# Kernel optimization log

Measured on AMD Instinct MI355X. Metric: run time of the kernel, lower is better.

The kernel has to match this reference:

```python
import jax, jax.numpy as jnp
import numpy as np

B, S, IN_DIM, OUT_DIM = 4, 2048, 1024, 1024
NEG = -9e15

def _xavier(key, shape, gain=1.414):
    fan_in, fan_out = shape[0], shape[1]
    a = gain * np.sqrt(6.0 / (fan_in + fan_out))
    return jax.random.uniform(key, shape, jnp.float32, -a, a)

def setup_inputs() -> dict:
    key = jax.random.key(0)
    ks = jax.random.split(key, 8)
    x = jax.random.normal(ks[0], (B, S, IN_DIM), jnp.float32)
    W_query = _xavier(ks[1], (IN_DIM, OUT_DIM))
    W_key = _xavier(ks[2], (IN_DIM, OUT_DIM))
    W_value = _xavier(ks[3], (IN_DIM, OUT_DIM))
    # torch Linear default init (kaiming-uniform-ish); values don't matter for correctness baseline
    W1 = _xavier(ks[4], (OUT_DIM + IN_DIM, OUT_DIM), gain=1.0)
    b1 = jnp.zeros((OUT_DIM,), jnp.float32)
    W2 = _xavier(ks[5], (OUT_DIM, OUT_DIM), gain=1.0)
    b2 = jnp.zeros((OUT_DIM,), jnp.float32)
    return {"x": x, "W_query": W_query, "W_key": W_key, "W_value": W_value,
            "W1": W1, "b1": b1, "W2": W2, "b2": b2}

def reference(x, W_query, W_key, W_value, W1, b1, W2, b2):
    # QKV projections: [B,S,in] @ [in,out] -> [B,S,out]
    q = jnp.einsum('bsi,io->bso', x, W_query)
    k = jnp.einsum('bsi,io->bso', x, W_key)
    v = jnp.einsum('bsi,io->bso', x, W_value)
    scale = 1.0 / jnp.sqrt(jnp.float32(OUT_DIM))
    e = jnp.einsum('bqd,bkd->bqk', q, k) * scale  # [B,S,S]
    causal = jnp.tril(jnp.ones((S, S), jnp.float32))  # mask > 0 keeps lower triangle
    attn = jnp.where(causal > 0, e, jnp.float32(NEG))
    attn = jax.nn.softmax(attn, axis=2)
    # dropout: eval mode (train=False) -> identity
    out = jnp.einsum('bqk,bkd->bqd', attn, v)  # [B,S,out]
    h = jnp.concatenate([out, x], axis=-1)  # [B,S,out+in]
    h = jax.nn.relu(jnp.einsum('bsf,fo->bso', h, W1) + b1)
    return jnp.einsum('bsf,fo->bso', h, W2) + b2
```

## Files before the change

kernel.cpp:

```cpp
#include <hip/hip_runtime.h>
#include <stdint.h>

typedef __attribute__((ext_vector_type(8))) short short8;
typedef __attribute__((ext_vector_type(4))) float f32x4;

__device__ __forceinline__ unsigned short f32_to_bf16(float f) {
    unsigned int u = __float_as_uint(f);
    u += 0x7FFFu + ((u >> 16) & 1u);
    return (unsigned short)(u >> 16);
}

__device__ __forceinline__ short8 load8_f32_as_bf16(const float* __restrict__ ap) {
    f32x4 f0 = *(const f32x4*)ap;
    f32x4 f1 = *(const f32x4*)(ap + 4);
    union { short8 s; unsigned short u[8]; } cv;
#pragma unroll
    for (int t = 0; t < 4; ++t) {
        cv.u[t]     = f32_to_bf16(f0[t]);
        cv.u[t + 4] = f32_to_bf16(f1[t]);
    }
    return cv.s;
}

__device__ __forceinline__ void gld_lds16(const void* g, void* l) {
    __builtin_amdgcn_global_load_lds(
        (const __attribute__((address_space(1))) unsigned int*)(unsigned long long)(uintptr_t)g,
        (__attribute__((address_space(3))) unsigned int*)(unsigned int)(uintptr_t)l,
        16, 0, 0);
}

__device__ __forceinline__ int triC(int y) {
    int t = y >> 1;
    return y + t * (t - 1) + ((y & 1) ? t : 0);
}

template<int AMODE, int EPI, int SWIZ, bool KLIMIT, int MT>
__global__ __launch_bounds__(256, 4)
void gemm128(const unsigned short* __restrict__ A, const unsigned short* __restrict__ A2,
             int lda, int lda2, int ksplit,
             const unsigned short* __restrict__ B, int ldb,
             void* __restrict__ C, int ldc, int K,
             long aStride, long bStride, long cStride,
             const float* __restrict__ bias, long biasStride, float scale,
             void* __restrict__ C2, int ldc2)
{
    int z = blockIdx.z;
    int mblk, nblk;
    if (SWIZ == 1) {
        int lin = blockIdx.y * gridDim.x + blockIdx.x;
        int mchunk = gridDim.y >> 3;
        int xcd = lin & 7, idx = lin >> 3;
        mblk = xcd * mchunk + idx % mchunk;
        nblk = idx / mchunk;
    } else if (SWIZ == 4) {
        mblk = (z & 2) ? ((int)gridDim.y - 1 - (int)blockIdx.y) : blockIdx.y;
        nblk = blockIdx.x;
    } else if (SWIZ == 5) {
        int x = blockIdx.x;
        int a = (int)(2.f * sqrtf((float)x));
        if (a > 31) a = 31;
        while (a < 31 && triC(a + 1) <= x) ++a;
        while (a > 0 && triC(a) > x) --a;
        mblk = a;
        nblk = x - triC(a);
    } else if (SWIZ == 6) {
        int x = blockIdx.x, yy = blockIdx.y;
        if (z < 2) { mblk = x * 8 + (yy & 7); nblk = yy >> 3; }
        else       { nblk = x * 8 + (yy & 7); mblk = yy >> 3; }
    } else {
        mblk = blockIdx.y;
        nblk = blockIdx.x;
    }
    int m0 = mblk * MT;
    int n0 = nblk * 128;

    const unsigned short* Ab;
    const unsigned short* Bb;
    if (SWIZ == 6) {
        if (z < 2) { Ab = A; Bb = B + (size_t)z * bStride; }
        else       { Ab = B + (size_t)2 * bStride; Bb = A; }
    } else {
        Ab = A + (size_t)z * aStride;
        Bb = B + (size_t)z * bStride;
    }

    __shared__ __align__(16) short As[MT * 64];
    __shared__ __align__(16) short Bs[128 * 64];

    int tid  = threadIdx.x;
    int lane = tid & 63, wid = tid >> 6;
    constexpr int MI = MT / 32;
    int wm = (wid & 1) * (MT / 2), wn = (wid >> 1) * 64;
    int fr = lane & 15, fq = lane >> 4;
    int sw0 = ((fq    ) ^ (fr & 7)) * 16;
    int sw1 = ((fq ^ 4) ^ (fr & 7)) * 16;

    int rS = tid >> 3;
    int cS = ((tid & 7) ^ (rS & 7)) * 8;
    char* AsB = (char*)As; char* BsB = (char*)Bs;

    int kend = KLIMIT ? min(K, m0 + MT) : K;

    f32x4 acc[MI][4];
#pragma unroll
    for (int i = 0; i < MI; ++i)
#pragma unroll
    for (int j = 0; j < 4; ++j) acc[i][j] = f32x4{0.f, 0.f, 0.f, 0.f};

    for (int k0 = 0; k0 < kend; k0 += 64) {
        const unsigned short* Asrc = Ab;
        int koff = k0, ldax = lda;
        if (AMODE == 2 && k0 >= ksplit) { Asrc = A2; koff = k0 - ksplit; ldax = lda2; }
        const unsigned short* pa = Asrc + (size_t)(m0 + rS) * ldax + koff + cS;
        const unsigned short* pb = Bb   + (size_t)(n0 + rS) * ldb  + k0   + cS;
#pragma unroll
        for (int t = 0; t < MT / 32; ++t)
            gld_lds16(pa + (size_t)(32 * t) * ldax, AsB + t * 4096 + tid * 16);
#pragma unroll
        for (int t = 0; t < 4; ++t)
            gld_lds16(pb + (size_t)(32 * t) * ldb,  BsB + t * 4096 + tid * 16);
        __syncthreads();

#pragma unroll
        for (int kh = 0; kh < 2; ++kh) {
            int sw = kh ? sw1 : sw0;
            short8 a[MI], b[4];
#pragma unroll
            for (int i = 0; i < MI; ++i)
                a[i] = *(const short8*)(AsB + (wm + i * 16 + fr) * 128 + sw);
#pragma unroll
            for (int j = 0; j < 4; ++j)
                b[j] = *(const short8*)(BsB + (wn + j * 16 + fr) * 128 + sw);
#pragma unroll
            for (int i = 0; i < MI; ++i)
#pragma unroll
            for (int j = 0; j < 4; ++j)
                acc[i][j] = __builtin_amdgcn_mfma_f32_16x16x32_bf16(a[i], b[j], acc[i][j], 0, 0, 0);
        }
        __syncthreads();
    }

    if (EPI == 0) {
        unsigned short* Cz; int ldcz;
        if (SWIZ == 6 && z >= 2) { Cz = (unsigned short*)C2; ldcz = ldc2; }
        else { Cz = (unsigned short*)C + (size_t)z * cStride; ldcz = ldc; }
#pragma unroll
        for (int i = 0; i < MI; ++i)
#pragma unroll
        for (int j = 0; j < 4; ++j)
#pragma unroll
        for (int r = 0; r < 4; ++r) {
            int row = m0 + wm + i * 16 + fq * 4 + r;
            int col = n0 + wn + j * 16 + fr;
            Cz[(size_t)row * ldcz + col] = f32_to_bf16(acc[i][j][r]);
        }
    } else if (EPI == 6) {
        unsigned short* Cz = (unsigned short*)C + (size_t)z * cStride;
        float* rs = const_cast<float*>(bias) + z * biasStride;
#pragma unroll
        for (int i = 0; i < MI; ++i)
#pragma unroll
        for (int r = 0; r < 4; ++r) {
            int row = m0 + wm + i * 16 + fq * 4 + r;
            float s = 0.f;
#pragma unroll
            for (int j = 0; j < 4; ++j) {
                int col = n0 + wn + j * 16 + fr;
                float e = (col <= row) ? __expf(acc[i][j][r] * scale - 16.f) : 0.f;
                s += e;
                Cz[(size_t)row * ldc + col] = f32_to_bf16(e);
            }
            s += __shfl_xor(s, 1);
            s += __shfl_xor(s, 2);
            s += __shfl_xor(s, 4);
            s += __shfl_xor(s, 8);
            if (fr == 0) atomicAdd(&rs[row], s);
        }
    } else if (EPI == 4) {
        unsigned short* Cz = (unsigned short*)C + (size_t)z * cStride;
#pragma unroll
        for (int i = 0; i < MI; ++i)
#pragma unroll
        for (int r = 0; r < 4; ++r) {
            int row = m0 + wm + i * 16 + fq * 4 + r;
            float inv = 1.f / bias[z * biasStride + row];
#pragma unroll
            for (int j = 0; j < 4; ++j) {
                int col = n0 + wn + j * 16 + fr;
                Cz[(size_t)row * ldc + col] = f32_to_bf16(acc[i][j][r] * inv);
            }
        }
    } else {
#pragma unroll
        for (int i = 0; i < MI; ++i)
#pragma unroll
        for (int j = 0; j < 4; ++j)
#pragma unroll
        for (int r = 0; r < 4; ++r) {
            int row = m0 + wm + i * 16 + fq * 4 + r;
            int col = n0 + wn + j * 16 + fr;
            float v = acc[i][j][r];
            if (EPI == 2) {
                v += bias[col];
                v = v > 0.f ? v : 0.f;
                ((unsigned short*)C + (size_t)z * cStride)[(size_t)row * ldc + col] = f32_to_bf16(v);
            } else {
                ((float*)C + (size_t)z * cStride)[(size_t)row * ldc + col] = v + bias[col];
            }
        }
    }
}

__device__ __forceinline__ void transpose_tile32(const float* __restrict__ in,
                                                 unsigned short* __restrict__ out,
                                                 int rows, int cols, int bx, int by, int tid)
{
    __shared__ float t[32][33];
    int tx = tid & 31, ty = tid >> 5;
    int r0 = by * 32, c0 = bx * 32;
#pragma unroll
    for (int i = 0; i < 4; ++i)
        t[ty + i * 8][tx] = in[(size_t)(r0 + ty + i * 8) * cols + c0 + tx];
    __syncthreads();
#pragma unroll
    for (int i = 0; i < 4; ++i)
        out[(size_t)(c0 + ty + i * 8) * rows + r0 + tx] = f32_to_bf16(t[tx][ty + i * 8]);
}

__global__ __launch_bounds__(256)
void prep_kernel(const float* __restrict__ x,
                 const float* __restrict__ Wq, const float* __restrict__ Wk,
                 const float* __restrict__ Wv, const float* __restrict__ W1,
                 const float* __restrict__ W2,
                 unsigned short* __restrict__ xb, unsigned short* __restrict__ WT,
                 unsigned short* __restrict__ W1T, unsigned short* __restrict__ W2T,
                 float* __restrict__ rsum)
{
    int idx = blockIdx.x;
    int tid = threadIdx.x;
    if (idx < 4096) {
        size_t i = ((size_t)idx * 256 + tid) * 8;
        *(short8*)(xb + i) = load8_f32_as_bf16(x + i);
    } else if (idx < 7168) {
        int t = idx - 4096;
        int w = t >> 10; t &= 1023;
        const float* in = w == 0 ? Wq : (w == 1 ? Wk : Wv);
        transpose_tile32(in, WT + (size_t)w * 1024 * 1024, 1024, 1024,
                         t & 31, t >> 5, tid);
    } else if (idx < 9216) {
        int t = idx - 7168;
        transpose_tile32(W1, W1T, 2048, 1024, t & 31, t >> 5, tid);
    } else if (idx < 10240) {
        int t = idx - 9216;
        transpose_tile32(W2, W2T, 1024, 1024, t & 31, t >> 5, tid);
    } else {
        int t = idx - 10240;
        f32x4 zero = {0.f, 0.f, 0.f, 0.f};
        float* p = rsum + ((size_t)t * 256 + tid) * 8;
        *(f32x4*)p = zero;
        *(f32x4*)(p + 4) = zero;
    }
}

extern "C" void kernel_launch(void* const* d_in, const int* in_sizes, int n_in,
                              void* d_out, int out_size, void* d_ws, size_t ws_size,
                              hipStream_t stream)
{
    const float* x  = (const float*)d_in[0];
    const float* Wq = (const float*)d_in[1];
    const float* Wk = (const float*)d_in[2];
    const float* Wv = (const float*)d_in[3];
    const float* W1 = (const float*)d_in[4];
    const float* b1 = (const float*)d_in[5];
    const float* W2 = (const float*)d_in[6];
    const float* b2 = (const float*)d_in[7];
    float* out = (float*)d_out;

    size_t off = 0;
    auto alloc = [&](size_t bytes) {
        char* r = (char*)d_ws + off;
        off += (bytes + 255) & ~(size_t)255;
        return r;
    };
    const size_t TOK = (size_t)8192 * 1024;
    unsigned short* WT   = (unsigned short*)alloc((size_t)3072 * 1024 * 2);
    unsigned short* W1T  = (unsigned short*)alloc((size_t)1024 * 2048 * 2);
    unsigned short* W2T  = (unsigned short*)alloc((size_t)1024 * 1024 * 2);
    unsigned short* xb   = (unsigned short*)alloc(TOK * 2);
    unsigned short* vT   = (unsigned short*)alloc((size_t)1024 * 8192 * 2);
    unsigned short* attn = (unsigned short*)alloc(TOK * 2);
    float*          rsum = (float*)         alloc((size_t)4 * 2048 * 4);
    unsigned short* q    = (unsigned short*)alloc(TOK * 2);
    unsigned short* k    = (unsigned short*)alloc(TOK * 2);
    unsigned short* S    = (unsigned short*)alloc((size_t)4 * 2048 * 2048 * 2);
    unsigned short* h1   = S;

    prep_kernel<<<10244, 256, 0, stream>>>(x, Wq, Wk, Wv, W1, W2, xb, WT, W1T, W2T, rsum);

    gemm128<0, 0, 6, false, 128><<<dim3(8, 64, 3), 256, 0, stream>>>(
        xb, nullptr, 1024, 0, 0, WT, 1024, q, 1024, 1024,
        0, (long)1024 * 1024, (long)TOK, nullptr, 0, 0.f, vT, 8192);

    gemm128<0, 6, 5, false, 64><<<dim3(272, 1, 4), 256, 0, stream>>>(
        q, nullptr, 1024, 0, 0, k, 1024, S, 2048, 1024,
        (long)2048 * 1024, (long)2048 * 1024, (long)2048 * 2048, rsum, 2048, 0.03125f,
        nullptr, 0);
    gemm128<0, 4, 4, true, 64><<<dim3(8, 32, 4), 256, 0, stream>>>(
        S, nullptr, 2048, 0, 0, vT, 8192, attn, 1024, 2048,
        (long)2048 * 2048, (long)2048, (long)2048 * 1024, rsum, 2048, 0.f, nullptr, 0);

    gemm128<2, 2, 1, false, 64><<<dim3(8, 128, 1), 256, 0, stream>>>(
        attn, xb, 1024, 1024, 1024, W1T, 2048, h1, 1024, 2048, 0, 0, 0, b1, 0, 0.f,
        nullptr, 0);
    gemm128<0, 3, 1, false, 64><<<dim3(8, 128, 1), 256, 0, stream>>>(
        h1, nullptr, 1024, 0, 0, W2T, 1024, out, 1024, 1024, 0, 0, 0, b2, 0, 0.f,
        nullptr, 0);
}
```

Before: 291.8 us.

## Add 256x128 eight-wave triple-buffered GEMM for QKV and MLP projections

Adds a new GEMM kernel with 512 threads, a 256x128 output tile and a three-slot LDS ring. Prefetch runs two K-steps ahead with one barrier per step, and setprio is raised around the MFMA block. The QKV projection and both MLP GEMMs now use it in place of the 128-tile kernel. The larger tile cuts global reloads and barrier overhead per FLOP, but it uses much more LDS, which may lower occupancy, and it leaves fewer blocks per grid.

```diff
diff --git a/kernel.cpp b/kernel.cpp
--- a/kernel.cpp
+++ b/kernel.cpp
@@ -211,6 +211,159 @@
     }
 }
 
+template<int AMODE, int EPI, int SWIZ>
+__global__ __launch_bounds__(512, 2)
+void gemm8p(const unsigned short* __restrict__ A, const unsigned short* __restrict__ A2,
+            int lda, int lda2, int ksplit,
+            const unsigned short* __restrict__ B, int ldb,
+            void* __restrict__ C, int ldc, int K,
+            long bStride, long cStride,
+            const float* __restrict__ bias,
+            void* __restrict__ C2, int ldc2)
+{
+    constexpr int BM = 256, BN = 128;
+    int z = blockIdx.z;
+    int lin = blockIdx.y * gridDim.x + blockIdx.x;
+    int xcd = lin & 7, idx = lin >> 3;
+    int mblk, nblk;
+    if (SWIZ == 6) {
+        if (z < 2) { mblk = xcd * 4 + (idx & 3); nblk = idx >> 2; }
+        else       { nblk = xcd * 8 + (idx & 7); mblk = idx >> 3; }
+    } else {
+        int mch = (int)gridDim.y >> 3;
+        mblk = xcd * mch + idx % mch;
+        nblk = idx / mch;
+    }
+    int m0 = mblk * BM, n0 = nblk * BN;
+
+    const unsigned short *Ab, *Bb;
+    if (SWIZ == 6) {
+        if (z < 2) { Ab = A; Bb = B + (size_t)z * bStride; }
+        else       { Ab = B + (size_t)2 * bStride; Bb = A; }
+    } else { Ab = A; Bb = B; }
+
+    constexpr int ATILE = BM * 64;
+    constexpr int BTILE = BN * 64;
+    constexpr int TILE  = ATILE + BTILE;
+    __shared__ __align__(16) short lds[3 * TILE];
+
+    int tid  = threadIdx.x;
+    int lane = tid & 63, wid = tid >> 6;
+    int wm = (wid & 3) * 64, wn = (wid >> 2) * 64;
+    int fr = lane & 15, fq = lane >> 4;
+    int sw0 = ((fq    ) ^ (fr & 7)) * 16;
+    int sw1 = ((fq ^ 4) ^ (fr & 7)) * 16;
+
+    int rS = tid >> 3;
+    int cS = ((tid & 7) ^ (rS & 7)) * 8;
+
+    int NT = K >> 6;
+
+    f32x4 acc[4][4];
+#pragma unroll
+    for (int i = 0; i < 4; ++i)
+#pragma unroll
+    for (int j = 0; j < 4; ++j) acc[i][j] = f32x4{0.f, 0.f, 0.f, 0.f};
+
+    auto STAGE = [&](int t, int slot) {
+        int k0 = t << 6;
+        char* dst = (char*)(lds + slot * TILE);
+        const unsigned short* Asrc = Ab; int koff = k0, ldax = lda;
+        if (AMODE == 2 && k0 >= ksplit) { Asrc = A2; koff = k0 - ksplit; ldax = lda2; }
+        const unsigned short* pa = Asrc + (size_t)(m0 + rS) * ldax + koff + cS;
+        const unsigned short* pb = Bb   + (size_t)(n0 + rS) * ldb  + k0   + cS;
+#pragma unroll
+        for (int u = 0; u < 4; ++u)
+            gld_lds16(pa + (size_t)(64 * u) * ldax, dst + u * 8192 + tid * 16);
+#pragma unroll
+        for (int u = 0; u < 2; ++u)
+            gld_lds16(pb + (size_t)(64 * u) * ldb, dst + 32768 + u * 8192 + tid * 16);
+    };
+
+    STAGE(0, 0);
+    STAGE(1, 1);
+    asm volatile("s_waitcnt vmcnt(6)" ::: "memory");
+    __builtin_amdgcn_s_barrier();
+    __builtin_amdgcn_sched_barrier(0);
+    asm volatile("" ::: "memory");
+
+    int sc = 0, ss = 2;
+    for (int t = 0; t < NT; ++t) {
+        if (t + 2 < NT) STAGE(t + 2, ss);
+        const char* AsB = (const char*)(lds + sc * TILE);
+        const char* BsB = AsB + 32768;
+#pragma unroll
+        for (int kh = 0; kh < 2; ++kh) {
+            int sw = kh ? sw1 : sw0;
+            short8 a[4], b[4];
+#pragma unroll
+            for (int i = 0; i < 4; ++i)
+                a[i] = *(const short8*)(AsB + (wm + i * 16 + fr) * 128 + sw);
+#pragma unroll
+            for (int j = 0; j < 4; ++j)
+                b[j] = *(const short8*)(BsB + (wn + j * 16 + fr) * 128 + sw);
+            __builtin_amdgcn_s_setprio(1);
+#pragma unroll
+            for (int i = 0; i < 4; ++i)
+#pragma unroll
+            for (int j = 0; j < 4; ++j)
+                acc[i][j] = __builtin_amdgcn_mfma_f32_16x16x32_bf16(a[i], b[j], acc[i][j], 0, 0, 0);
+            __builtin_amdgcn_s_setprio(0);
+        }
+        if (t + 1 < NT) {
+            if (t + 2 < NT) { asm volatile("s_waitcnt vmcnt(6)" ::: "memory"); }
+            else            { asm volatile("s_waitcnt vmcnt(0)" ::: "memory"); }
+            __builtin_amdgcn_s_barrier();
+            __builtin_amdgcn_sched_barrier(0);
+            asm volatile("" ::: "memory");
+        }
+        sc = sc == 2 ? 0 : sc + 1;
+        ss = ss == 2 ? 0 : ss + 1;
+    }
+
+    if (EPI == 0) {
+        unsigned short* Cz; int ldcz;
+        if (SWIZ == 6 && z >= 2) { Cz = (unsigned short*)C2; ldcz = ldc2; }
+        else { Cz = (unsigned short*)C + (size_t)z * cStride; ldcz = ldc; }
+#pragma unroll
+        for (int i = 0; i < 4; ++i)
+#pragma unroll
+        for (int j = 0; j < 4; ++j)
+#pragma unroll
+        for (int r = 0; r < 4; ++r) {
+            int row = m0 + wm + i * 16 + fq * 4 + r;
+            int col = n0 + wn + j * 16 + fr;
+            Cz[(size_t)row * ldcz + col] = f32_to_bf16(acc[i][j][r]);
+        }
+    } else if (EPI == 2) {
+        unsigned short* Cz = (unsigned short*)C;
+#pragma unroll
+        for (int i = 0; i < 4; ++i)
+#pragma unroll
+        for (int j = 0; j < 4; ++j)
+#pragma unroll
+        for (int r = 0; r < 4; ++r) {
+            int row = m0 + wm + i * 16 + fq * 4 + r;
+            int col = n0 + wn + j * 16 + fr;
+            float v = acc[i][j][r] + bias[col];
+            v = v > 0.f ? v : 0.f;
+            Cz[(size_t)row * ldc + col] = f32_to_bf16(v);
+        }
+    } else {
+        float* Cz = (float*)C;
+#pragma unroll
+        for (int i = 0; i < 4; ++i)
+#pragma unroll
+        for (int j = 0; j < 4; ++j)
+#pragma unroll
+        for (int r = 0; r < 4; ++r) {
+            int row = m0 + wm + i * 16 + fq * 4 + r;
+            int col = n0 + wn + j * 16 + fr;
+            Cz[(size_t)row * ldc + col] = acc[i][j][r] + bias[col];
+        }
+    }
+}
+
 __device__ __forceinline__ void transpose_tile32(const float* __restrict__ in,
                                                  unsigned short* __restrict__ out,
                                                  int rows, int cols, int bx, int by, int tid)
@@ -297,9 +450,9 @@
 
     prep_kernel<<<10244, 256, 0, stream>>>(x, Wq, Wk, Wv, W1, W2, xb, WT, W1T, W2T, rsum);
 
-    gemm128<0, 0, 6, false, 128><<<dim3(8, 64, 3), 256, 0, stream>>>(
+    gemm8p<0, 0, 6><<<dim3(4, 64, 3), 512, 0, stream>>>(
         xb, nullptr, 1024, 0, 0, WT, 1024, q, 1024, 1024,
-        0, (long)1024 * 1024, (long)TOK, nullptr, 0, 0.f, vT, 8192);
+        (long)1024 * 1024, (long)TOK, nullptr, vT, 8192);
 
     gemm128<0, 6, 5, false, 64><<<dim3(272, 1, 4), 256, 0, stream>>>(
         q, nullptr, 1024, 0, 0, k, 1024, S, 2048, 1024,
@@ -309,10 +462,10 @@
         S, nullptr, 2048, 0, 0, vT, 8192, attn, 1024, 2048,
         (long)2048 * 2048, (long)2048, (long)2048 * 1024, rsum, 2048, 0.f, nullptr, 0);
 
-    gemm128<2, 2, 1, false, 64><<<dim3(8, 128, 1), 256, 0, stream>>>(
-        attn, xb, 1024, 1024, 1024, W1T, 2048, h1, 1024, 2048, 0, 0, 0, b1, 0, 0.f,
-        nullptr, 0);
-    gemm128<0, 3, 1, false, 64><<<dim3(8, 128, 1), 256, 0, stream>>>(
-        h1, nullptr, 1024, 0, 0, W2T, 1024, out, 1024, 1024, 0, 0, 0, b2, 0, 0.f,
-        nullptr, 0);
-}
+    gemm8p<2, 2, 1><<<dim3(8, 32, 1), 512, 0, stream>>>(
+        attn, xb, 1024, 1024, 1024, W1T, 2048, h1, 1024, 2048,
+        0, 0, b1, nullptr, 0);
+    gemm8p<0, 3, 1><<<dim3(8, 32, 1), 512, 0, stream>>>(
+        h1, nullptr, 1024, 0, 0, W2T, 1024, out, 1024, 1024,
+        0, 0, b2, nullptr, 0);
+}
```

Result: no change. 291.0 us (-0.2%).
